# Kernel optimization log

Measured on AMD Instinct MI355X. Metric: run time of the kernel, lower is better.

The kernel has to match this reference:

```python
import jax, jax.numpy as jnp
import numpy as np

NUM_HEADS = 4
NUM_GROUPS = 32
EPS = 1e-5


def setup_inputs() -> dict:
    key = jax.random.key(0)
    ks = jax.random.split(key, 4)
    ch = 256
    x = jax.random.normal(ks[0], (16, ch, 32, 32), dtype=jnp.float32)
    gn_w = jnp.ones((ch,), jnp.float32)
    gn_b = jnp.zeros((ch,), jnp.float32)
    # conv1x1 weights, kaiming-ish scale
    qkv_w = jax.random.normal(ks[1], (3 * ch, ch), dtype=jnp.float32) / np.sqrt(ch)
    qkv_b = jnp.zeros((3 * ch,), jnp.float32)
    proj_w = jax.random.normal(ks[2], (ch, ch), dtype=jnp.float32) / np.sqrt(ch)
    proj_b = jnp.zeros((ch,), jnp.float32)
    return {"x": x, "gn_w": gn_w, "gn_b": gn_b, "qkv_w": qkv_w,
            "qkv_b": qkv_b, "proj_w": proj_w, "proj_b": proj_b}


def _group_norm(x, w, b):
    bsz, c, h, wd = x.shape
    g = NUM_GROUPS
    xg = x.reshape(bsz, g, c // g, h, wd)
    mean = xg.mean(axis=(2, 3, 4), keepdims=True)
    var = xg.var(axis=(2, 3, 4), keepdims=True)
    xg = (xg - mean) * jax.lax.rsqrt(var + EPS)
    return xg.reshape(bsz, c, h, wd) * w[None, :, None, None] + b[None, :, None, None]


def reference(x, gn_w, gn_b, qkv_w, qkv_b, proj_w, proj_b):
    b, c, h, w = x.shape
    hd = c // NUM_HEADS
    scale = hd ** (-0.5)
    y = _group_norm(x, gn_w, gn_b)
    # 1x1 conv == channel matmul
    qkv = jnp.einsum('oc,bchw->bohw', qkv_w, y) + qkv_b[None, :, None, None]
    q, k, v = jnp.split(qkv, 3, axis=1)
    q = q.reshape(b, NUM_HEADS, hd, h * w)
    k = k.reshape(b, NUM_HEADS, hd, h * w)
    v = v.reshape(b, NUM_HEADS, hd, h * w)
    attn = jnp.einsum('bhdi,bhdj->bhij', q * scale, k)
    attn = jax.nn.softmax(attn, axis=-1)
    out = jnp.einsum('bhij,bhdj->bhdi', attn, v)
    out = out.reshape(b, c, h, w)
    out = jnp.einsum('oc,bchw->bohw', proj_w, out) + proj_b[None, :, None, None]
    return x + out
```

## Files before the change

### kernel.cpp

```cpp
#include <hip/hip_runtime.h>
#include <cstddef>

#define B_   16
#define C_   256
#define HW_  1024
#define NH_  4
#define NG_  32
#define CPG_ 8
#define CS_  0.18033688f

typedef __attribute__((ext_vector_type(8))) short bf16x8;
typedef __attribute__((ext_vector_type(4))) short s16x4;
typedef __attribute__((ext_vector_type(8))) _Float16 f16x8;
typedef __attribute__((ext_vector_type(4))) float f32x4;

#define MFMA16B(a, b, c) __builtin_amdgcn_mfma_f32_16x16x32_bf16(a, b, c, 0, 0, 0)
#define MFMA16H(a, b, c) __builtin_amdgcn_mfma_f32_16x16x32_f16(a, b, c, 0, 0, 0)

#if __has_builtin(__builtin_amdgcn_mfma_f32_16x16x16bf16_1k)
#define HAVE_MFMA16K16 1
#define MFMA16B4(a, b, c) __builtin_amdgcn_mfma_f32_16x16x16bf16_1k(a, b, c, 0, 0, 0)
#else
#define HAVE_MFMA16K16 0
#endif

__device__ __forceinline__ float bf2f(unsigned short h) {
    unsigned int u = ((unsigned int)h) << 16;
    return __builtin_bit_cast(float, u);
}
__device__ __forceinline__ unsigned short f2bf(float f) {
    unsigned int u = __builtin_bit_cast(unsigned int, f);
    u += 0x7FFFu + ((u >> 16) & 1u);
    return (unsigned short)(u >> 16);
}
#if __has_builtin(__builtin_amdgcn_cvt_pk_bf16_f32)
__device__ __forceinline__ unsigned packbf(float a, float b) {
    auto v = __builtin_amdgcn_cvt_pk_bf16_f32(a, b);
    return __builtin_bit_cast(unsigned, v);
}
#else
__device__ __forceinline__ unsigned packbf(float a, float b) {
    unsigned ua = __builtin_bit_cast(unsigned, a) + 0x8000u;
    unsigned ub = __builtin_bit_cast(unsigned, b) + 0x8000u;
    return __builtin_amdgcn_perm(ub, ua, 0x07060302u);
}
#endif
__device__ __forceinline__ unsigned pkh(float a, float b) {
    auto h2 = __builtin_amdgcn_cvt_pkrtz(a, b);
    return __builtin_bit_cast(unsigned, h2);
}

__global__ __launch_bounds__(256) void gn_wcvt_kernel(
    const float* __restrict__ x,
    const float* __restrict__ gw,
    const float* __restrict__ gb,
    unsigned short* __restrict__ y16,
    const float* __restrict__ qw, const float* __restrict__ pw,
    unsigned short* __restrict__ oq, unsigned short* __restrict__ op)
{
    if (blockIdx.x >= 512) {
        int i = (blockIdx.x - 512) * 256 + threadIdx.x;
        const float* s; unsigned short* d; int j;
        if (i < 49152) { s = qw; d = oq; j = i; }
        else           { s = pw; d = op; j = i - 49152; }
        float4 f = ((const float4*)s)[j];
        uint2 u = {pkh(f.x, f.y), pkh(f.z, f.w)};
        *(uint2*)&d[(size_t)j * 4] = u;
        return;
    }
    int blk = blockIdx.x;
    const size_t base = (size_t)blk * CPG_ * HW_;
    const float* xg = x + base;
    const int N = CPG_ * HW_;

    float s = 0.f, ss = 0.f;
    for (int e = threadIdx.x * 4; e < N; e += 1024) {
        float4 v4 = *(const float4*)&xg[e];
        s  += v4.x + v4.y + v4.z + v4.w;
        ss += v4.x * v4.x + v4.y * v4.y + v4.z * v4.z + v4.w * v4.w;
    }
    #pragma unroll
    for (int off = 32; off > 0; off >>= 1) {
        s  += __shfl_down(s, off, 64);
        ss += __shfl_down(ss, off, 64);
    }
    __shared__ float red[8];
    __shared__ float2 stf;
    int lane = threadIdx.x & 63, wv = threadIdx.x >> 6;
    if (lane == 0) { red[wv] = s; red[4 + wv] = ss; }
    __syncthreads();
    if (threadIdx.x == 0) {
        float S  = red[0] + red[1] + red[2] + red[3];
        float SS = red[4] + red[5] + red[6] + red[7];
        float mean = S / (float)N;
        float var  = SS / (float)N - mean * mean;
        stf = make_float2(mean, rsqrtf(var + 1e-5f));
    }
    __syncthreads();
    float mean = stf.x, rstd = stf.y;
    for (int e = threadIdx.x * 4; e < N; e += 1024) {
        int ch = (blk & 31) * CPG_ + (e >> 10);
        float sc = rstd * gw[ch];
        float sh = gb[ch] - mean * sc;
        float4 v4 = *(const float4*)&xg[e];
        uint2 u;
        u.x = pkh(v4.x * sc + sh, v4.y * sc + sh);
        u.y = pkh(v4.z * sc + sh, v4.w * sc + sh);
        *(uint2*)&y16[base + e] = u;
    }
}

__global__ __launch_bounds__(256) void qkv_mfma_kernel(
    const unsigned short* __restrict__ W16,
    const unsigned short* __restrict__ y16,
    const float* __restrict__ bias,
    unsigned short* __restrict__ qT,
    unsigned short* __restrict__ kT,
    unsigned short* __restrict__ vN)
{
    const int K = 256, N = 1024;
    __shared__ union {
        struct { unsigned short A[2][128][40]; unsigned short Bt[2][64][40]; } st;
        unsigned short nd[2][64][72];
        unsigned short mn[128][72];
    } L;

    const int b  = blockIdx.z;
    const int m0 = blockIdx.y * 128, n0 = blockIdx.x * 64;
    const int t  = threadIdx.x;
    const int l15 = t & 15, quad = (t >> 4) & 3;
    const int wave = t >> 6, wm = wave >> 1, wn = wave & 1;

    union HF { uint4 q; f16x8 v; };

    f32x4 acc[4][2];
    #pragma unroll
    for (int mt = 0; mt < 4; ++mt)
        #pragma unroll
        for (int nt = 0; nt < 2; ++nt)
            acc[mt][nt] = (f32x4){0.f, 0.f, 0.f, 0.f};

    const int ar = t >> 1, akh = (t & 1) * 16;
    const int bn = t & 63, bkb = t >> 6;

    uint4 pa0, pa1;
    unsigned short ph[8];

    auto PREF = [&](int k0) {
        const unsigned short* wp = &W16[(size_t)(m0 + ar) * K + k0 + akh];
        pa0 = *(const uint4*)wp;
        pa1 = *(const uint4*)(wp + 8);
        int ch = k0 + bkb * 8;
        const unsigned short* xp = &y16[((size_t)b * 256 + ch) * 1024 + n0 + bn];
        #pragma unroll
        for (int j = 0; j < 8; ++j) ph[j] = xp[(size_t)j * 1024];
    };

    PREF(0);
    #pragma unroll 1
    for (int it = 0; it < 8; ++it) {
        const int bsel = it & 1;
        *(uint4*)&L.st.A[bsel][ar][akh]     = pa0;
        *(uint4*)&L.st.A[bsel][ar][akh + 8] = pa1;
        {
            uint4 bw;
            bw.x = (unsigned)ph[0] | ((unsigned)ph[1] << 16);
            bw.y = (unsigned)ph[2] | ((unsigned)ph[3] << 16);
            bw.z = (unsigned)ph[4] | ((unsigned)ph[5] << 16);
            bw.w = (unsigned)ph[6] | ((unsigned)ph[7] << 16);
            *(uint4*)&L.st.Bt[bsel][bn][bkb * 8] = bw;
        }
        __syncthreads();
        if (it + 1 < 8) PREF((it + 1) * 32);
        HF af[4], bfv[2];
        #pragma unroll
        for (int mt = 0; mt < 4; ++mt)
            af[mt].q = *(const uint4*)&L.st.A[bsel][wm * 64 + mt * 16 + l15][quad * 8];
        #pragma unroll
        for (int nt = 0; nt < 2; ++nt)
            bfv[nt].q = *(const uint4*)&L.st.Bt[bsel][wn * 32 + nt * 16 + l15][quad * 8];
        #pragma unroll
        for (int mt = 0; mt < 4; ++mt)
            #pragma unroll
            for (int nt = 0; nt < 2; ++nt)
                acc[mt][nt] = MFMA16H(af[mt].v, bfv[nt].v, acc[mt][nt]);
    }
    __syncthreads();

    if (m0 < 512) {
        const float qsc = (m0 < 256) ? CS_ : 1.f;
        #pragma unroll
        for (int mt = 0; mt < 4; ++mt)
            #pragma unroll
            for (int rr = 0; rr < 4; ++rr) {
                int dl = mt * 16 + quad * 4 + rr;
                float bv = bias[m0 + wm * 64 + dl];
                #pragma unroll
                for (int nt = 0; nt < 2; ++nt)
                    L.nd[wm][wn * 32 + nt * 16 + l15][dl] = f2bf((acc[mt][nt][rr] + bv) * qsc);
            }
        __syncthreads();
        unsigned short* dst = (m0 < 256) ? qT : kT;
        int headbase = (m0 & 255) >> 6;
        int hl = t >> 7, tt = t & 127;
        int nl = tt >> 1, db = (tt & 1) * 32;
        const unsigned short* src = &L.nd[hl][nl][db];
        unsigned short* gp = &dst[(((size_t)(b * 4 + headbase + hl)) * 1024 + n0 + nl) * 64 + db];
        uint4 u0 = *(const uint4*)(src);
        uint4 u1 = *(const uint4*)(src + 8);
        uint4 u2 = *(const uint4*)(src + 16);
        uint4 u3 = *(const uint4*)(src + 24);
        *(uint4*)(gp)      = u0;
        *(uint4*)(gp + 8)  = u1;
        *(uint4*)(gp + 16) = u2;
        *(uint4*)(gp + 24) = u3;
    } else {
        #pragma unroll
        for (int mt = 0; mt < 4; ++mt)
            #pragma unroll
            for (int rr = 0; rr < 4; ++rr) {
                int ml = wm * 64 + mt * 16 + quad * 4 + rr;
                float bv = bias[m0 + ml];
                #pragma unroll
                for (int nt = 0; nt < 2; ++nt)
                    L.mn[ml][wn * 32 + nt * 16 + l15] = f2bf(acc[mt][nt][rr] + bv);
            }
        __syncthreads();
        int ml = t & 127, nb = t >> 7;
        const unsigned short* src = &L.mn[ml][nb * 32];
        unsigned short* gp = &vN[((size_t)b * 256 + (m0 - 512) + ml) * 1024 + n0 + nb * 32];
        uint4 u0 = *(const uint4*)(src);
        uint4 u1 = *(const uint4*)(src + 8);
        uint4 u2 = *(const uint4*)(src + 16);
        uint4 u3 = *(const uint4*)(src + 24);
        *(uint4*)(gp)      = u0;
        *(uint4*)(gp + 8)  = u1;
        *(uint4*)(gp + 16) = u2;
        *(uint4*)(gp + 24) = u3;
    }
}

__global__ __launch_bounds__(256) void proj_mfma_kernel(
    const unsigned short* __restrict__ W16,
    const unsigned short* __restrict__ OP,
    const float* __restrict__ LPp,
    const float* __restrict__ bias,
    const float* __restrict__ res,
    float* __restrict__ outF)
{
    const int M = 256, K = 256, N = 1024;
    __shared__ struct { unsigned short A[2][64][40]; unsigned short Bt[2][64][40]; } L;

    const int b  = blockIdx.z;
    const int m0 = blockIdx.y * 64, n0 = blockIdx.x * 64;
    const int t  = threadIdx.x;
    const int l15 = t & 15, quad = (t >> 4) & 3;
    const int wave = t >> 6, wm = wave >> 1, wn = wave & 1;

    union HF { uint4 q; f16x8 v; };

    f32x4 acc[2][2];
    #pragma unroll
    for (int mt = 0; mt < 2; ++mt)
        #pragma unroll
        for (int nt = 0; nt < 2; ++nt)
            acc[mt][nt] = (f32x4){0.f, 0.f, 0.f, 0.f};

    const int ar = t >> 2, akh = (t & 3) * 8;
    const int bn = t & 63, bkb = t >> 6;

    float rinv[4];
    {
        int n = n0 + bn;
        #pragma unroll
        for (int h = 0; h < 4; ++h) {
            float l0 = LPp[(size_t)(b * 4 + h) * 1024 + n];
            float l1 = LPp[(size_t)(64 + b * 4 + h) * 1024 + n];
            rinv[h] = 1.f / (l0 + l1);
        }
    }

    uint4 pa;
    unsigned short ph0[8], ph1[8];
    int pH = 0;

    auto PREF = [&](int k0) {
        pa = *(const uint4*)&W16[(size_t)(m0 + ar) * K + k0 + akh];
        int ch = k0 + bkb * 8;
        pH = ch >> 6;
        size_t base = ((size_t)(b * 4 + pH) * 64 + (ch & 63)) * 1024 + n0 + bn;
        #pragma unroll
        for (int j = 0; j < 8; ++j) {
            ph0[j] = OP[base + (size_t)j * 1024];
            ph1[j] = OP[(size_t)64 * 64 * 1024 + base + (size_t)j * 1024];
        }
    };

    PREF(0);
    #pragma unroll 1
    for (int it = 0; it < 8; ++it) {
        const int bsel = it & 1;
        *(uint4*)&L.A[bsel][ar][akh] = pa;
        {
            float ri = rinv[pH];
            float v[8];
            #pragma unroll
            for (int j = 0; j < 8; ++j)
                v[j] = (bf2f(ph0[j]) + bf2f(ph1[j])) * ri;
            uint4 bw = {pkh(v[0], v[1]), pkh(v[2], v[3]), pkh(v[4], v[5]), pkh(v[6], v[7])};
            *(uint4*)&L.Bt[bsel][bn][bkb * 8] = bw;
        }
        __syncthreads();
        if (it + 1 < 8) PREF((it + 1) * 32);
        HF af[2], bfv[2];
        #pragma unroll
        for (int mt = 0; mt < 2; ++mt)
            af[mt].q = *(const uint4*)&L.A[bsel][wm * 32 + mt * 16 + l15][quad * 8];
        #pragma unroll
        for (int nt = 0; nt < 2; ++nt)
            bfv[nt].q = *(const uint4*)&L.Bt[bsel][wn * 32 + nt * 16 + l15][quad * 8];
        #pragma unroll
        for (int mt = 0; mt < 2; ++mt)
            #pragma unroll
            for (int nt = 0; nt < 2; ++nt)
                acc[mt][nt] = MFMA16H(af[mt].v, bfv[nt].v, acc[mt][nt]);
    }

    #pragma unroll
    for (int mt = 0; mt < 2; ++mt) {
        #pragma unroll
        for (int rr = 0; rr < 4; ++rr) {
            int m = m0 + wm * 32 + mt * 16 + quad * 4 + rr;
            float bv = bias[m];
            #pragma unroll
            for (int nt = 0; nt < 2; ++nt) {
                int n = n0 + wn * 32 + nt * 16 + l15;
                size_t off = ((size_t)b * M + m) * (size_t)N + n;
                outF[off] = acc[mt][nt][rr] + bv + res[off];
            }
        }
    }
}

__global__ __launch_bounds__(256) void attn_mfma_kernel(
    const unsigned short* __restrict__ qT,
    const unsigned short* __restrict__ kT,
    const unsigned short* __restrict__ vN,
    unsigned short* __restrict__ OP,
    float* __restrict__ LP)
{
    __shared__ unsigned short Kt[2][64][72];
    __shared__ unsigned short Vs[2][64][72];

    const int t    = threadIdx.x;
    const int wv   = t >> 6;
    const int l15  = t & 15;
    const int quad = (t >> 4) & 3;
    const int bh   = blockIdx.x;
    const int i0   = blockIdx.y * 128;
    const int jh   = blockIdx.z;

    union FragU { uint4 q; unsigned u[4]; bf16x8 v; };

    FragU qf[2][2];
    {
        const unsigned short* qg = qT + (size_t)bh * (1024 * 64);
        int qrow = i0 + wv * 32 + l15;
        #pragma unroll
        for (int nt = 0; nt < 2; ++nt)
            #pragma unroll
            for (int kt = 0; kt < 2; ++kt)
                qf[nt][kt].q = *(const uint4*)&qg[(size_t)(qrow + nt * 16) * 64 + kt * 32 + quad * 8];
    }

    f32x4 accO[4][2];
    #pragma unroll
    for (int m = 0; m < 4; ++m)
        #pragma unroll
        for (int n = 0; n < 2; ++n)
            accO[m][n] = (f32x4){0.f, 0.f, 0.f, 0.f};
    float l_i[2] = {0.f, 0.f};
#if HAVE_MFMA16K16
    f32x4 accL[2] = {(f32x4){0.f, 0.f, 0.f, 0.f}, (f32x4){0.f, 0.f, 0.f, 0.f}};
    const s16x4 ones4 = {(short)0x3F80, (short)0x3F80, (short)0x3F80, (short)0x3F80};
#endif

    const unsigned short* kg = kT + (size_t)bh * (1024 * 64);
    const unsigned short* vg = vN + (size_t)bh * (64 * 1024);

    const int slbase = l15 + ((quad & 1) << 5);
    const bool upper = (t & 32) != 0;
    (void)slbase; (void)upper;
    const int sr = t >> 2, sc = (t & 3) * 16;

    uint4 kr0, kr1, vr0, vr1;
    {
        const int j0 = jh * 512;
        const unsigned short* kp = &kg[(size_t)(j0 + sr) * 64 + sc];
        const unsigned short* vp = &vg[(size_t)sr * 1024 + j0 + sc];
        kr0 = *(const uint4*)kp;  kr1 = *(const uint4*)(kp + 8);
        vr0 = *(const uint4*)vp;  vr1 = *(const uint4*)(vp + 8);
    }

    for (int it = 0; it < 8; ++it) {
        const int bsel = it & 1;
        *(uint4*)&Kt[bsel][sr][sc]     = kr0;
        *(uint4*)&Kt[bsel][sr][sc + 8] = kr1;
        *(uint4*)&Vs[bsel][sr][sc]     = vr0;
        *(uint4*)&Vs[bsel][sr][sc + 8] = vr1;
        __syncthreads();
        if (it < 7) {
            const int j0n = jh * 512 + (it + 1) * 64;
            const unsigned short* kp = &kg[(size_t)(j0n + sr) * 64 + sc];
            const unsigned short* vp = &vg[(size_t)sr * 1024 + j0n + sc];
            kr0 = *(const uint4*)kp;  kr1 = *(const uint4*)(kp + 8);
            vr0 = *(const uint4*)vp;  vr1 = *(const uint4*)(vp + 8);
        }

        f32x4 accS[4][2];
        #pragma unroll
        for (int mt = 0; mt < 4; ++mt) {
            FragU ak[2];
            #pragma unroll
            for (int kt = 0; kt < 2; ++kt)
                ak[kt].q = *(const uint4*)&Kt[bsel][mt * 16 + l15][kt * 32 + quad * 8];
            #pragma unroll
            for (int nt = 0; nt < 2; ++nt) {
                f32x4 z = (f32x4){0.f, 0.f, 0.f, 0.f};
                z = MFMA16B(ak[0].v, qf[nt][0].v, z);
                z = MFMA16B(ak[1].v, qf[nt][1].v, z);
                accS[mt][nt] = z;
            }
        }

#if HAVE_MFMA16K16
        union PB { unsigned u[2]; s16x4 v; };
        PB pb[4][2];
        #pragma unroll
        for (int mt = 0; mt < 4; ++mt)
            #pragma unroll
            for (int nt = 0; nt < 2; ++nt) {
                float p0 = exp2f(accS[mt][nt][0]);
                float p1 = exp2f(accS[mt][nt][1]);
                float p2 = exp2f(accS[mt][nt][2]);
                float p3 = exp2f(accS[mt][nt][3]);
                pb[mt][nt].u[0] = packbf(p0, p1);
                pb[mt][nt].u[1] = packbf(p2, p3);
            }
        #pragma unroll
        for (int mt = 0; mt < 4; ++mt)
            #pragma unroll
            for (int nt = 0; nt < 2; ++nt)
                accL[nt] = MFMA16B4(ones4, pb[mt][nt].v, accL[nt]);
        #pragma unroll
        for (int mtd = 0; mtd < 4; ++mtd) {
            union AV { uint2 d; s16x4 v; } av[4];
            #pragma unroll
            for (int mt = 0; mt < 4; ++mt)
                av[mt].d = *(const uint2*)&Vs[bsel][mtd * 16 + l15][mt * 16 + quad * 4];
            #pragma unroll
            for (int nt = 0; nt < 2; ++nt)
                #pragma unroll
                for (int mt = 0; mt < 4; ++mt)
                    accO[mtd][nt] = MFMA16B4(av[mt].v, pb[mt][nt].v, accO[mtd][nt]);
        }
#else
        float rs[2] = {0.f, 0.f};
        unsigned pk[4][2][2];
        #pragma unroll
        for (int mt = 0; mt < 4; ++mt)
            #pragma unroll
            for (int nt = 0; nt < 2; ++nt) {
                float p0 = exp2f(accS[mt][nt][0]);
                float p1 = exp2f(accS[mt][nt][1]);
                float p2 = exp2f(accS[mt][nt][2]);
                float p3 = exp2f(accS[mt][nt][3]);
                rs[nt] += (p0 + p1) + (p2 + p3);
                pk[mt][nt][0] = packbf(p0, p1);
                pk[mt][nt][1] = packbf(p2, p3);
            }
        #pragma unroll
        for (int nt = 0; nt < 2; ++nt) {
            float r = rs[nt];
            r += __shfl_xor(r, 16, 64);
            r += __shfl_xor(r, 32, 64);
            l_i[nt] += r;
        }
        FragU bfr[2][2];
        #pragma unroll
        for (int kt = 0; kt < 2; ++kt)
            #pragma unroll
            for (int nt = 0; nt < 2; ++nt)
                #pragma unroll
                for (int w4 = 0; w4 < 4; ++w4) {
                    int sl = slbase + ((w4 >> 1) << 4);
                    int lo = __shfl((int)pk[2 * kt + 0][nt][w4 & 1], sl, 64);
                    int hi = __shfl((int)pk[2 * kt + 1][nt][w4 & 1], sl, 64);
                    bfr[kt][nt].u[w4] = (unsigned)(upper ? hi : lo);
                }
        #pragma unroll
        for (int mtd = 0; mtd < 4; ++mtd) {
            FragU av[2];
            #pragma unroll
            for (int kt = 0; kt < 2; ++kt)
                av[kt].q = *(const uint4*)&Vs[bsel][mtd * 16 + l15][kt * 32 + quad * 8];
            #pragma unroll
            for (int nt = 0; nt < 2; ++nt) {
                accO[mtd][nt] = MFMA16B(av[0].v, bfr[0][nt].v, accO[mtd][nt]);
                accO[mtd][nt] = MFMA16B(av[1].v, bfr[1][nt].v, accO[mtd][nt]);
            }
        }
#endif
    }

#if HAVE_MFMA16K16
    l_i[0] = accL[0][0];
    l_i[1] = accL[1][0];
#endif

    unsigned short* ob = OP + ((size_t)jh * 64 + bh) * (64 * 1024) + i0 + wv * 32;
    #pragma unroll
    for (int mtd = 0; mtd < 4; ++mtd)
        #pragma unroll
        for (int nt = 0; nt < 2; ++nt)
            #pragma unroll
            for (int rr = 0; rr < 4; ++rr) {
                int d = mtd * 16 + quad * 4 + rr;
                ob[(size_t)d * 1024 + nt * 16 + l15] = f2bf(accO[mtd][nt][rr]);
            }
    if (quad == 0) {
        float* lp = &LP[((size_t)jh * 64 + bh) * 1024 + i0 + wv * 32 + l15];
        lp[0]  = l_i[0];
        lp[16] = l_i[1];
    }
}

extern "C" void kernel_launch(void* const* d_in, const int* in_sizes, int n_in,
                              void* d_out, int out_size, void* d_ws, size_t ws_size,
                              hipStream_t stream)
{
    const float* x      = (const float*)d_in[0];
    const float* gn_w   = (const float*)d_in[1];
    const float* gn_b   = (const float*)d_in[2];
    const float* qkv_w  = (const float*)d_in[3];
    const float* qkv_b  = (const float*)d_in[4];
    const float* proj_w = (const float*)d_in[5];
    const float* proj_b = (const float*)d_in[6];
    float* out = (float*)d_out;

    char* ws = (char*)d_ws;
    unsigned short* y16  = (unsigned short*)ws;
    unsigned short* w16q = y16 + (size_t)B_ * C_ * HW_;
    unsigned short* w16p = w16q + 768 * 256;
    unsigned short* qT   = w16p + 256 * 256;
    unsigned short* kT   = qT + (size_t)B_ * NH_ * HW_ * 64;
    unsigned short* vN   = kT + (size_t)B_ * NH_ * HW_ * 64;
    unsigned short* OP   = vN + (size_t)B_ * C_ * HW_;
    float*          LP   = (float*)(OP + (size_t)2 * B_ * C_ * HW_);
    (void)in_sizes; (void)n_in; (void)out_size; (void)ws_size;

    gn_wcvt_kernel<<<dim3(768), 256, 0, stream>>>(
        x, gn_w, gn_b, y16, qkv_w, proj_w, w16q, w16p);

    qkv_mfma_kernel<<<dim3(HW_ / 64, 6, B_), 256, 0, stream>>>(
        w16q, y16, qkv_b, qT, kT, vN);

    attn_mfma_kernel<<<dim3(NH_ * B_, HW_ / 128, 2), 256, 0, stream>>>(qT, kT, vN, OP, LP);

    proj_mfma_kernel<<<dim3(HW_ / 64, C_ / 64, B_), 256, 0, stream>>>(
        w16p, OP, LP, proj_b, x, out);
}
```

Before: 147.6 us.

## Halve attention query tile per block and single-buffer K/V shared memory

Each attention block now handles 64 query rows instead of 128, with each wave owning 16 rows, and the launch grid doubles along the query dimension. K/V shared memory drops from double to single buffering, and a trailing barrier is added to protect the reused buffer. This cuts per-thread registers and LDS, which should allow more waves per CU and more blocks in flight. In exchange, every K/V tile is loaded from global memory twice as often, and each iteration now takes an extra barrier.

```diff
diff --git a/kernel.cpp b/kernel.cpp
--- a/kernel.cpp
+++ b/kernel.cpp
@@ -349,39 +349,34 @@
     unsigned short* __restrict__ OP,
     float* __restrict__ LP)
 {
-    __shared__ unsigned short Kt[2][64][72];
-    __shared__ unsigned short Vs[2][64][72];
+    __shared__ unsigned short Kt[64][72];
+    __shared__ unsigned short Vs[64][72];
 
     const int t    = threadIdx.x;
     const int wv   = t >> 6;
     const int l15  = t & 15;
     const int quad = (t >> 4) & 3;
     const int bh   = blockIdx.x;
-    const int i0   = blockIdx.y * 128;
+    const int i0   = blockIdx.y * 64;
     const int jh   = blockIdx.z;
 
     union FragU { uint4 q; unsigned u[4]; bf16x8 v; };
 
-    FragU qf[2][2];
+    FragU qf[2];
     {
         const unsigned short* qg = qT + (size_t)bh * (1024 * 64);
-        int qrow = i0 + wv * 32 + l15;
-        #pragma unroll
-        for (int nt = 0; nt < 2; ++nt)
-            #pragma unroll
-            for (int kt = 0; kt < 2; ++kt)
-                qf[nt][kt].q = *(const uint4*)&qg[(size_t)(qrow + nt * 16) * 64 + kt * 32 + quad * 8];
-    }
-
-    f32x4 accO[4][2];
+        int qrow = i0 + wv * 16 + l15;
+        #pragma unroll
+        for (int kt = 0; kt < 2; ++kt)
+            qf[kt].q = *(const uint4*)&qg[(size_t)qrow * 64 + kt * 32 + quad * 8];
+    }
+
+    f32x4 accO[4];
     #pragma unroll
-    for (int m = 0; m < 4; ++m)
-        #pragma unroll
-        for (int n = 0; n < 2; ++n)
-            accO[m][n] = (f32x4){0.f, 0.f, 0.f, 0.f};
-    float l_i[2] = {0.f, 0.f};
+    for (int m = 0; m < 4; ++m) accO[m] = (f32x4){0.f, 0.f, 0.f, 0.f};
+    float l_i = 0.f;
 #if HAVE_MFMA16K16
-    f32x4 accL[2] = {(f32x4){0.f, 0.f, 0.f, 0.f}, (f32x4){0.f, 0.f, 0.f, 0.f}};
+    f32x4 accL = (f32x4){0.f, 0.f, 0.f, 0.f};
     const s16x4 ones4 = {(short)0x3F80, (short)0x3F80, (short)0x3F80, (short)0x3F80};
 #endif
 
@@ -403,11 +398,10 @@
     }
 
     for (int it = 0; it < 8; ++it) {
-        const int bsel = it & 1;
-        *(uint4*)&Kt[bsel][sr][sc]     = kr0;
-        *(uint4*)&Kt[bsel][sr][sc + 8] = kr1;
-        *(uint4*)&Vs[bsel][sr][sc]     = vr0;
-        *(uint4*)&Vs[bsel][sr][sc + 8] = vr1;
+        *(uint4*)&Kt[sr][sc]     = kr0;
+        *(uint4*)&Kt[sr][sc + 8] = kr1;
+        *(uint4*)&Vs[sr][sc]     = vr0;
+        *(uint4*)&Vs[sr][sc + 8] = vr1;
         __syncthreads();
         if (it < 7) {
             const int j0n = jh * 512 + (it + 1) * 64;
@@ -417,122 +411,97 @@
             vr0 = *(const uint4*)vp;  vr1 = *(const uint4*)(vp + 8);
         }
 
-        f32x4 accS[4][2];
+        f32x4 accS[4];
         #pragma unroll
         for (int mt = 0; mt < 4; ++mt) {
             FragU ak[2];
             #pragma unroll
             for (int kt = 0; kt < 2; ++kt)
-                ak[kt].q = *(const uint4*)&Kt[bsel][mt * 16 + l15][kt * 32 + quad * 8];
-            #pragma unroll
-            for (int nt = 0; nt < 2; ++nt) {
-                f32x4 z = (f32x4){0.f, 0.f, 0.f, 0.f};
-                z = MFMA16B(ak[0].v, qf[nt][0].v, z);
-                z = MFMA16B(ak[1].v, qf[nt][1].v, z);
-                accS[mt][nt] = z;
-            }
+                ak[kt].q = *(const uint4*)&Kt[mt * 16 + l15][kt * 32 + quad * 8];
+            f32x4 z = (f32x4){0.f, 0.f, 0.f, 0.f};
+            z = MFMA16B(ak[0].v, qf[0].v, z);
+            z = MFMA16B(ak[1].v, qf[1].v, z);
+            accS[mt] = z;
         }
 
 #if HAVE_MFMA16K16
         union PB { unsigned u[2]; s16x4 v; };
-        PB pb[4][2];
+        PB pb[4];
+        #pragma unroll
+        for (int mt = 0; mt < 4; ++mt) {
+            float p0 = exp2f(accS[mt][0]);
+            float p1 = exp2f(accS[mt][1]);
+            float p2 = exp2f(accS[mt][2]);
+            float p3 = exp2f(accS[mt][3]);
+            pb[mt].u[0] = packbf(p0, p1);
+            pb[mt].u[1] = packbf(p2, p3);
+        }
         #pragma unroll
         for (int mt = 0; mt < 4; ++mt)
-            #pragma unroll
-            for (int nt = 0; nt < 2; ++nt) {
-                float p0 = exp2f(accS[mt][nt][0]);
-                float p1 = exp2f(accS[mt][nt][1]);
-                float p2 = exp2f(accS[mt][nt][2]);
-                float p3 = exp2f(accS[mt][nt][3]);
-                pb[mt][nt].u[0] = packbf(p0, p1);
-                pb[mt][nt].u[1] = packbf(p2, p3);
-            }
-        #pragma unroll
-        for (int mt = 0; mt < 4; ++mt)
-            #pragma unroll
-            for (int nt = 0; nt < 2; ++nt)
-                accL[nt] = MFMA16B4(ones4, pb[mt][nt].v, accL[nt]);
+            accL = MFMA16B4(ones4, pb[mt].v, accL);
         #pragma unroll
         for (int mtd = 0; mtd < 4; ++mtd) {
             union AV { uint2 d; s16x4 v; } av[4];
             #pragma unroll
             for (int mt = 0; mt < 4; ++mt)
-                av[mt].d = *(const uint2*)&Vs[bsel][mtd * 16 + l15][mt * 16 + quad * 4];
-            #pragma unroll
-            for (int nt = 0; nt < 2; ++nt)
-                #pragma unroll
-                for (int mt = 0; mt < 4; ++mt)
-                    accO[mtd][nt] = MFMA16B4(av[mt].v, pb[mt][nt].v, accO[mtd][nt]);
+                av[mt].d = *(const uint2*)&Vs[mtd * 16 + l15][mt * 16 + quad * 4];
+            #pragma unroll
+            for (int mt = 0; mt < 4; ++mt)
+                accO[mtd] = MFMA16B4(av[mt].v, pb[mt].v, accO[mtd]);
         }
 #else
-        float rs[2] = {0.f, 0.f};
-        unsigned pk[4][2][2];
-        #pragma unroll
-        for (int mt = 0; mt < 4; ++mt)
-            #pragma unroll
-            for (int nt = 0; nt < 2; ++nt) {
-                float p0 = exp2f(accS[mt][nt][0]);
-                float p1 = exp2f(accS[mt][nt][1]);
-                float p2 = exp2f(accS[mt][nt][2]);
-                float p3 = exp2f(accS[mt][nt][3]);
-                rs[nt] += (p0 + p1) + (p2 + p3);
-                pk[mt][nt][0] = packbf(p0, p1);
-                pk[mt][nt][1] = packbf(p2, p3);
+        float rs = 0.f;
+        unsigned pk[4][2];
+        #pragma unroll
+        for (int mt = 0; mt < 4; ++mt) {
+            float p0 = exp2f(accS[mt][0]);
+            float p1 = exp2f(accS[mt][1]);
+            float p2 = exp2f(accS[mt][2]);
+            float p3 = exp2f(accS[mt][3]);
+            rs += (p0 + p1) + (p2 + p3);
+            pk[mt][0] = packbf(p0, p1);
+            pk[mt][1] = packbf(p2, p3);
+        }
+        rs += __shfl_xor(rs, 16, 64);
+        rs += __shfl_xor(rs, 32, 64);
+        l_i += rs;
+        FragU bfr[2];
+        #pragma unroll
+        for (int kt = 0; kt < 2; ++kt)
+            #pragma unroll
+            for (int w4 = 0; w4 < 4; ++w4) {
+                int sl = slbase + ((w4 >> 1) << 4);
+                int lo = __shfl((int)pk[2 * kt + 0][w4 & 1], sl, 64);
+                int hi = __shfl((int)pk[2 * kt + 1][w4 & 1], sl, 64);
+                bfr[kt].u[w4] = (unsigned)(upper ? hi : lo);
             }
-        #pragma unroll
-        for (int nt = 0; nt < 2; ++nt) {
-            float r = rs[nt];
-            r += __shfl_xor(r, 16, 64);
-            r += __shfl_xor(r, 32, 64);
-            l_i[nt] += r;
-        }
-        FragU bfr[2][2];
-        #pragma unroll
-        for (int kt = 0; kt < 2; ++kt)
-            #pragma unroll
-            for (int nt = 0; nt < 2; ++nt)
-                #pragma unroll
-                for (int w4 = 0; w4 < 4; ++w4) {
-                    int sl = slbase + ((w4 >> 1) << 4);
-                    int lo = __shfl((int)pk[2 * kt + 0][nt][w4 & 1], sl, 64);
-                    int hi = __shfl((int)pk[2 * kt + 1][nt][w4 & 1], sl, 64);
-                    bfr[kt][nt].u[w4] = (unsigned)(upper ? hi : lo);
-                }
         #pragma unroll
         for (int mtd = 0; mtd < 4; ++mtd) {
             FragU av[2];
             #pragma unroll
             for (int kt = 0; kt < 2; ++kt)
-                av[kt].q = *(const uint4*)&Vs[bsel][mtd * 16 + l15][kt * 32 + quad * 8];
-            #pragma unroll
-            for (int nt = 0; nt < 2; ++nt) {
-                accO[mtd][nt] = MFMA16B(av[0].v, bfr[0][nt].v, accO[mtd][nt]);
-                accO[mtd][nt] = MFMA16B(av[1].v, bfr[1][nt].v, accO[mtd][nt]);
-            }
+                av[kt].q = *(const uint4*)&Vs[mtd * 16 + l15][kt * 32 + quad * 8];
+            accO[mtd] = MFMA16B(av[0].v, bfr[0].v, accO[mtd]);
+            accO[mtd] = MFMA16B(av[1].v, bfr[1].v, accO[mtd]);
         }
 #endif
+        __syncthreads();
     }
 
 #if HAVE_MFMA16K16
-    l_i[0] = accL[0][0];
-    l_i[1] = accL[1][0];
+    l_i = accL[0];
 #endif
 
-    unsigned short* ob = OP + ((size_t)jh * 64 + bh) * (64 * 1024) + i0 + wv * 32;
+    unsigned short* ob = OP + ((size_t)jh * 64 + bh) * (64 * 1024) + i0 + wv * 16;
     #pragma unroll
     for (int mtd = 0; mtd < 4; ++mtd)
         #pragma unroll
-        for (int nt = 0; nt < 2; ++nt)
-            #pragma unroll
-            for (int rr = 0; rr < 4; ++rr) {
-                int d = mtd * 16 + quad * 4 + rr;
-                ob[(size_t)d * 1024 + nt * 16 + l15] = f2bf(accO[mtd][nt][rr]);
-            }
-    if (quad == 0) {
-        float* lp = &LP[((size_t)jh * 64 + bh) * 1024 + i0 + wv * 32 + l15];
-        lp[0]  = l_i[0];
-        lp[16] = l_i[1];
-    }
+        for (int rr = 0; rr < 4; ++rr) {
+            int d = mtd * 16 + quad * 4 + rr;
+            ob[(size_t)d * 1024 + l15] = f2bf(accO[mtd][rr]);
+        }
+    if (quad == 0)
+        LP[((size_t)jh * 64 + bh) * 1024 + i0 + wv * 16 + l15] = l_i;
 }
 
 extern "C" void kernel_launch(void* const* d_in, const int* in_sizes, int n_in,
@@ -565,7 +534,7 @@
     qkv_mfma_kernel<<<dim3(HW_ / 64, 6, B_), 256, 0, stream>>>(
         w16q, y16, qkv_b, qT, kT, vN);
 
-    attn_mfma_kernel<<<dim3(NH_ * B_, HW_ / 128, 2), 256, 0, stream>>>(qT, kT, vN, OP, LP);
+    attn_mfma_kernel<<<dim3(NH_ * B_, HW_ / 64, 2), 256, 0, stream>>>(qT, kT, vN, OP, LP);
 
     proj_mfma_kernel<<<dim3(HW_ / 64, C_ / 64, B_), 256, 0, stream>>>(
         w16p, OP, LP, proj_b, x, out);
```

Result: no change. 147.9 us, median of 2 (+0.2%).
